# Optimization experiments

Measured on AMD Instinct MI355X. Metric: run time of the kernel, lower is better.

## Reference

```python
import jax, jax.numpy as jnp
import numpy as np

N, LT, LV, D, H = 4, 1024, 1024, 1024, 16
HD = D // H
EPS = 1e-12


def layernorm(x, w, b):
    u = x.mean(-1, keepdims=True)
    s = ((x - u) ** 2).mean(-1, keepdims=True)
    return w * (x - u) / jnp.sqrt(s + EPS) + b


def attention(q_in, k_in, v_in, mask, qw, qb, kw, kb, vw, vb):
    # mask: (N, Lq_or_1, Lk) float in {0,1}; torch Linear is x @ W.T + b
    def heads(x, w, b):
        y = x @ w.T + b
        return y.reshape(y.shape[0], y.shape[1], H, HD).transpose(0, 2, 1, 3)  # (N,H,L,hd)
    q, k, v = heads(q_in, qw, qb), heads(k_in, kw, kb), heads(v_in, vw, vb)
    scores = jnp.einsum('bhqd,bhkd->bhqk', q, k) / np.sqrt(HD).astype(np.float32)
    scores = scores + (1.0 - mask[:, None]) * (-10000.0)
    probs = jax.nn.softmax(scores, axis=-1)  # dropout is identity in eval
    ctx = jnp.einsum('bhqk,bhkd->bhqd', probs, v)
    return ctx.transpose(0, 2, 1, 3).reshape(q_in.shape[0], q_in.shape[1], D)


def setup_inputs() -> dict:
    key = jax.random.key(0)
    ks = jax.random.split(key, 16)
    inp = {
        'dec_hidden_states': jax.random.normal(ks[0], (N, LT, D), jnp.float32),
        'enc_outputs': jax.random.normal(ks[1], (N, LV, D), jnp.float32),
        'dec_mask': jnp.ones((N, LT), jnp.float32),
        'enc_mask': jnp.ones((N, LV), jnp.float32),
    }
    wnames = ['sa_qw', 'sa_kw', 'sa_vw', 'ca_qw', 'ca_kw', 'ca_vw', 'out_w']
    for i, n in enumerate(wnames):
        inp[n] = jax.random.normal(ks[2 + i], (D, D), jnp.float32) * 0.02
    for n in ['sa_qb', 'sa_kb', 'sa_vb', 'ca_qb', 'ca_kb', 'ca_vb', 'out_b', 'n1_b', 'n2_b', 'out_ln_b']:
        inp[n] = jnp.zeros((D,), jnp.float32)
    for n in ['n1_w', 'n2_w', 'out_ln_w']:
        inp[n] = jnp.ones((D,), jnp.float32)
    return inp


def reference(dec_hidden_states, enc_outputs, dec_mask, enc_mask,
              sa_qw, sa_qb, sa_kw, sa_kb, sa_vw, sa_vb, n1_w, n1_b,
              ca_qw, ca_qb, ca_kw, ca_kb, ca_vw, ca_vb, n2_w, n2_b,
              out_w, out_b, out_ln_w, out_ln_b):
    Lt = dec_mask.shape[1]
    # diagonal_mask=True: causal tril combined with padding mask
    self_mask = dec_mask[:, None, :] * jnp.tril(jnp.ones((Lt, Lt), dec_mask.dtype))  # (N,Lt,Lt)
    a = attention(dec_hidden_states, dec_hidden_states, dec_hidden_states, self_mask,
                  sa_qw, sa_qb, sa_kw, sa_kb, sa_vw, sa_vb)
    a = layernorm(a + dec_hidden_states, n1_w, n1_b)
    c = attention(a, enc_outputs, enc_outputs, enc_mask[:, None, :],
                  ca_qw, ca_qb, ca_kw, ca_kb, ca_vw, ca_vb)
    c = layernorm(a + c, n2_w, n2_b)
    # BertOutput called as output(x, x): dense, residual, LN (dropout = identity)
    h = c @ out_w.T + out_b
    return layernorm(h + c, out_ln_w, out_ln_b)
```

## Files before the change

kernel.cpp:

```cpp
#include <hip/hip_runtime.h>
#include <cstdint>
#include <cstddef>

typedef __bf16 bf16x8 __attribute__((ext_vector_type(8)));
typedef float  floatx4 __attribute__((ext_vector_type(4)));
typedef unsigned short ushortx8 __attribute__((ext_vector_type(8)));
typedef unsigned short ushortx4 __attribute__((ext_vector_type(4)));

#define MFMA16(a, b, c) __builtin_amdgcn_mfma_f32_16x16x32_bf16((a), (b), (c), 0, 0, 0)

__device__ inline unsigned short f2bf(float f) {
    unsigned int u = __float_as_uint(f);
    unsigned int r = (u + 0x7fffu + ((u >> 16) & 1u)) >> 16;
    return (unsigned short)r;
}

struct Src2 { const float* p[2]; };
__global__ __launch_bounds__(256) void k_x2_to_bf16(Src2 s2, unsigned short* __restrict__ dst) {
    int i = blockIdx.x * 256 + threadIdx.x;
    const float* src = s2.p[i >> 19];
    int off = i & 524287;
    const float4* s = (const float4*)src + (size_t)off * 2;
    float4 x0 = s[0], x1 = s[1];
    ushortx8 o;
    o[0] = f2bf(x0.x); o[1] = f2bf(x0.y); o[2] = f2bf(x0.z); o[3] = f2bf(x0.w);
    o[4] = f2bf(x1.x); o[5] = f2bf(x1.y); o[6] = f2bf(x1.z); o[7] = f2bf(x1.w);
    *((ushortx8*)dst + i) = o;
}
struct Src7 { const float* p[7]; };
__global__ __launch_bounds__(256) void k_w7_to_bf16(Src7 s7, unsigned short* __restrict__ dst) {
    int i = blockIdx.x * 256 + threadIdx.x;
    const float* src = s7.p[i >> 17];
    int off = i & 131071;
    const float4* s = (const float4*)src + (size_t)off * 2;
    float4 x0 = s[0], x1 = s[1];
    ushortx8 o;
    o[0] = f2bf(x0.x); o[1] = f2bf(x0.y); o[2] = f2bf(x0.z); o[3] = f2bf(x0.w);
    o[4] = f2bf(x1.x); o[5] = f2bf(x1.y); o[6] = f2bf(x1.z); o[7] = f2bf(x1.w);
    *((ushortx8*)dst + i) = o;
}

template <int MODE>
__global__ __launch_bounds__(256) void k_gemm_bias(const unsigned short* __restrict__ A,
                                                   const unsigned short* __restrict__ A2,
                                                   const unsigned short* __restrict__ W,
                                                   const float* __restrict__ bias0,
                                                   const float* __restrict__ bias1,
                                                   const float* __restrict__ bias2,
                                                   void* __restrict__ d0,
                                                   void* __restrict__ d1,
                                                   void* __restrict__ d2,
                                                   int K) {
    __shared__ __align__(16) unsigned short As[128 * 64];
    __shared__ __align__(16) unsigned short Bs[128 * 64];
    const int tid = threadIdx.x;
    const int wave = tid >> 6, lane = tid & 63;
    const int quad = lane >> 4, l15 = lane & 15;
    const int wm = wave >> 1, wn = wave & 1;

    constexpr int NT = (MODE == 3) ? 8 : 24;
    int fid = blockIdx.y * 32 + blockIdx.x;
    int xcd = fid & 7, idx = fid >> 3;
    const int m0 = (xcd * 4 + idx / NT) * 128;
    const int n0 = (idx % NT) * 128;
    const int sect_blk = n0 >> 10;

    const unsigned short* Ause = (MODE == 4 && sect_blk != 0) ? A2 : A;

    const size_t rowbytes = (size_t)K * 2;
    const int idx0 = tid, idx1 = 256 + tid;
    const char* pA0 = (const char*)Ause + (size_t)(m0 + (idx0 >> 2)) * rowbytes + ((idx0 & 3) << 4);
    const char* pA1 = (const char*)Ause + (size_t)(m0 + (idx1 >> 2)) * rowbytes + ((idx1 & 3) << 4);
    const char* pB0 = (const char*)W + (size_t)(n0 + (idx0 >> 2)) * rowbytes + ((idx0 & 3) << 4);
    const char* pB1 = (const char*)W + (size_t)(n0 + (idx1 >> 2)) * rowbytes + ((idx1 & 3) << 4);

    int4 a0a = *(const int4*)pA0, a0b = *(const int4*)(pA0 + 64);
    int4 a1a = *(const int4*)pA1, a1b = *(const int4*)(pA1 + 64);
    int4 b0a = *(const int4*)pB0, b0b = *(const int4*)(pB0 + 64);
    int4 b1a = *(const int4*)pB1, b1b = *(const int4*)(pB1 + 64);

    floatx4 acc[4][4] = {};

    const int KT = K >> 6;
    for (int kt = 0; kt < KT; ++kt) {
        __syncthreads();
        ((int4*)As)[idx0] = a0a; ((int4*)As)[idx1] = a1a;
        ((int4*)As)[512 + idx0] = a0b; ((int4*)As)[512 + idx1] = a1b;
        ((int4*)Bs)[idx0] = b0a; ((int4*)Bs)[idx1] = b1a;
        ((int4*)Bs)[512 + idx0] = b0b; ((int4*)Bs)[512 + idx1] = b1b;
        __syncthreads();
        if (kt + 1 < KT) {
            pA0 += 128; pA1 += 128; pB0 += 128; pB1 += 128;
            a0a = *(const int4*)pA0; a0b = *(const int4*)(pA0 + 64);
            a1a = *(const int4*)pA1; a1b = *(const int4*)(pA1 + 64);
            b0a = *(const int4*)pB0; b0b = *(const int4*)(pB0 + 64);
            b1a = *(const int4*)pB1; b1b = *(const int4*)(pB1 + 64);
        }
        const char* Asb = (const char*)As;
        const char* Bsb = (const char*)Bs;
#pragma unroll
        for (int half = 0; half < 2; ++half) {
            const int hb = half * 8192;
            bf16x8 af[4], bfr[4];
#pragma unroll
            for (int r = 0; r < 4; ++r)
                af[r] = *(const bf16x8*)(Asb + hb + ((wm * 64 + r * 16 + l15) * 64 + quad * 16));
#pragma unroll
            for (int c = 0; c < 4; ++c)
                bfr[c] = *(const bf16x8*)(Bsb + hb + ((wn * 64 + c * 16 + l15) * 64 + quad * 16));
#pragma unroll
            for (int r = 0; r < 4; ++r)
#pragma unroll
                for (int c = 0; c < 4; ++c)
                    acc[r][c] = MFMA16(af[r], bfr[c], acc[r][c]);
        }
    }

#pragma unroll
    for (int c = 0; c < 4; ++c) {
        int col = n0 + wn * 64 + c * 16 + l15;
        int sect = col >> 10, cc = col & 1023;
        float bv;
        if (MODE == 3) bv = bias0[col];
        else bv = (sect == 0 ? bias0 : (sect == 1 ? bias1 : bias2))[cc];
        int h = cc >> 6, d = cc & 63;
#pragma unroll
        for (int r = 0; r < 4; ++r) {
            int mrow = m0 + wm * 64 + r * 16 + quad * 4;
#pragma unroll
            for (int i = 0; i < 4; ++i) {
                float v = acc[r][c][i] + bv;
                int row = mrow + i;
                if (MODE == 3) {
                    ((float*)d0)[(size_t)row * 1024 + col] = v;
                } else {
                    int b = row >> 10, l = row & 1023;
                    unsigned short* base = (unsigned short*)(sect == 0 ? d0 : (sect == 1 ? d1 : d2));
                    bool isV = (sect == 2);
                    size_t off;
                    if (isV) {
                        int kk = l & 31;
                        off = (size_t)(b * 16 + h) * 65536 + (size_t)(l >> 5) * 2048 + d * 32 + kk;
                    } else {
                        off = ((size_t)(b * 16 + h) * 1024 + l) * 64 + d;
                    }
                    base[off] = f2bf(v);
                }
            }
        }
    }
}

__global__ __launch_bounds__(256, 4) void k_flash_attn(const unsigned short* __restrict__ Qp,
                                                       const unsigned short* __restrict__ Kp,
                                                       const unsigned short* __restrict__ Vp,
                                                       const float* __restrict__ mask,
                                                       float* __restrict__ ctx,
                                                       int causal) {
    const int L = 1024, D = 1024;
    const float SC = 0.18033688011112042f;
    int f = blockIdx.x;
    int g = f >> 7;
    int qsel = (f >> 3) & 15;
    int bh = (f & 7) + (g << 3);
    int qt = (qsel + 2 * g) & 15;
    int h = bh & 15, b = bh >> 4;
    int tid = threadIdx.x;
    int wave = tid >> 6, lane = tid & 63, quad = lane >> 4, l15 = lane & 15;
    int qbase = qt * 64 + wave * 16;

    __shared__ __align__(16) unsigned short Ks[2 * 4096];
    __shared__ __align__(16) unsigned short Vs[2 * 5120];
    __shared__ float penf[1024];

    {
        float4 mv = ((const float4*)(mask + b * L))[tid];
        float4 pv;
        pv.x = (1.0f - mv.x) * -14426.950408889634f;
        pv.y = (1.0f - mv.y) * -14426.950408889634f;
        pv.z = (1.0f - mv.z) * -14426.950408889634f;
        pv.w = (1.0f - mv.w) * -14426.950408889634f;
        ((float4*)penf)[tid] = pv;
    }

    const unsigned short* Qh = Qp + ((size_t)(b * 16 + h) * 1024 + qbase) * 64;
    bf16x8 qf0 = *(const bf16x8*)(Qh + l15 * 64 + quad * 8);
    bf16x8 qf1 = *(const bf16x8*)(Qh + l15 * 64 + 32 + quad * 8);

    const char* Kh = (const char*)(Kp + (size_t)(b * 16 + h) * 65536);
    const char* Vh = (const char*)(Vp + (size_t)(b * 16 + h) * 65536);

    int ktiles = causal ? (qt + 1) : 16;

    int krow = tid >> 3, kblk = tid & 7;
    int kd0 = krow * 128 + ((kblk ^ (krow & 7)) << 4);
    int kd1 = kd0 + 4096;
    int vd0 = (tid >> 2) * 80 + ((tid & 3) << 4);
    int vd1 = vd0 + 5120;

    int karA[4], karB[4];
#pragma unroll
    for (int r = 0; r < 4; ++r) {
        int row = r * 16 + l15;
        karA[r] = row * 128 + ((quad ^ (l15 & 7)) << 4);
        karB[r] = row * 128 + (((quad | 4) ^ (l15 & 7)) << 4);
    }
    int var_[8];
#pragma unroll
    for (int s = 0; s < 2; ++s)
#pragma unroll
        for (int fi = 0; fi < 4; ++fi)
            var_[s * 4 + fi] = s * 5120 + (fi * 16 + l15) * 80 + (quad << 4);

    floatx4 O[4] = {};
    float lsum = 0.0f;

    int4 ka0 = *(const int4*)(Kh + tid * 16);
    int4 ka1 = *(const int4*)(Kh + 4096 + tid * 16);
    int4 va0 = *(const int4*)(Vh + tid * 16);
    int4 va1 = *(const int4*)(Vh + 4096 + tid * 16);
    {
        char* Kw = (char*)Ks;
        char* Vw = (char*)Vs;
        *(int4*)(Kw + kd0) = ka0;
        *(int4*)(Kw + kd1) = ka1;
        *(int4*)(Vw + vd0) = va0;
        *(int4*)(Vw + vd1) = va1;
    }
    __syncthreads();

    for (int kt = 0; kt < ktiles; ++kt) {
        const char* Ksb = (const char*)Ks + (size_t)(kt & 1) * 8192;
        const char* Vsb = (const char*)Vs + (size_t)(kt & 1) * 10240;
        int k0 = kt * 64;
        bool last = (kt + 1 >= ktiles);

        bf16x8 kA[4], kB[4];
#pragma unroll
        for (int r = 0; r < 4; ++r) {
            kA[r] = *(const bf16x8*)(Ksb + karA[r]);
            kB[r] = *(const bf16x8*)(Ksb + karB[r]);
        }
        bf16x8 vv[8];
#pragma unroll
        for (int s = 0; s < 8; ++s) vv[s] = *(const bf16x8*)(Vsb + var_[s]);

        if (!last) {
            const char* Kg = Kh + (size_t)(kt + 1) * 8192;
            const char* Vg = Vh + (size_t)(kt + 1) * 8192;
            ka0 = *(const int4*)(Kg + tid * 16);
            ka1 = *(const int4*)(Kg + 4096 + tid * 16);
            va0 = *(const int4*)(Vg + tid * 16);
            va1 = *(const int4*)(Vg + 4096 + tid * 16);
        }

        floatx4 T[4] = {};
        T[0] = MFMA16(kA[0], qf0, T[0]); T[0] = MFMA16(kB[0], qf1, T[0]);
        T[1] = MFMA16(kA[1], qf0, T[1]); T[1] = MFMA16(kB[1], qf1, T[1]);
        T[2] = MFMA16(kA[2], qf0, T[2]); T[2] = MFMA16(kB[2], qf1, T[2]);
        T[3] = MFMA16(kA[3], qf0, T[3]); T[3] = MFMA16(kB[3], qf1, T[3]);

        bool boundary = causal && (kt == ktiles - 1);
        int qv = qbase + l15;

        unsigned w_[4][2];
#pragma unroll
        for (int s = 0; s < 4; ++s) {
            floatx4 pr = *(const floatx4*)(penf + k0 + 16 * s + quad * 4);
            unsigned rr[4];
#pragma unroll
            for (int i = 0; i < 4; ++i) {
                float x = fmaf(T[s][i], SC, pr[i]);
                if (boundary) {
                    int key = k0 + 16 * s + quad * 4 + i;
                    x = (key <= qv) ? x : -50000.0f;
                }
                float p = __builtin_amdgcn_exp2f(x);
                lsum += p;
                rr[i] = __float_as_uint(p) + 0x8000u;
            }
            w_[s][0] = __builtin_amdgcn_perm(rr[1], rr[0], 0x07060302u);
            w_[s][1] = __builtin_amdgcn_perm(rr[3], rr[2], 0x07060302u);
        }

        unsigned a00 = w_[0][0], a10 = w_[1][0];
        unsigned a01 = w_[0][1], a11 = w_[1][1];
        unsigned a20 = w_[2][0], a30 = w_[3][0];
        unsigned a21 = w_[2][1], a31 = w_[3][1];
        asm("v_permlane32_swap_b32 %0, %1" : "+v"(a00), "+v"(a10));
        asm("v_permlane32_swap_b32 %0, %1" : "+v"(a01), "+v"(a11));
        asm("v_permlane32_swap_b32 %0, %1" : "+v"(a20), "+v"(a30));
        asm("v_permlane32_swap_b32 %0, %1" : "+v"(a21), "+v"(a31));
        asm("v_permlane16_swap_b32 %0, %1" : "+v"(a00), "+v"(a10));
        asm("v_permlane16_swap_b32 %0, %1" : "+v"(a01), "+v"(a11));
        asm("v_permlane16_swap_b32 %0, %1" : "+v"(a20), "+v"(a30));
        asm("v_permlane16_swap_b32 %0, %1" : "+v"(a21), "+v"(a31));
        union PU { unsigned u[4]; bf16x8 v; };
        PU pl, ph;
        pl.u[0] = a00; pl.u[1] = a01; pl.u[2] = a10; pl.u[3] = a11;
        ph.u[0] = a20; ph.u[1] = a21; ph.u[2] = a30; ph.u[3] = a31;

        O[0] = MFMA16(pl.v, vv[0], O[0]);
        O[1] = MFMA16(pl.v, vv[1], O[1]);
        O[2] = MFMA16(pl.v, vv[2], O[2]);
        O[3] = MFMA16(pl.v, vv[3], O[3]);
        O[0] = MFMA16(ph.v, vv[4], O[0]);
        O[1] = MFMA16(ph.v, vv[5], O[1]);
        O[2] = MFMA16(ph.v, vv[6], O[2]);
        O[3] = MFMA16(ph.v, vv[7], O[3]);

        if (!last) {
            char* Kw = (char*)Ks + (size_t)((kt + 1) & 1) * 8192;
            char* Vw = (char*)Vs + (size_t)((kt + 1) & 1) * 10240;
            *(int4*)(Kw + kd0) = ka0;
            *(int4*)(Kw + kd1) = ka1;
            *(int4*)(Vw + vd0) = va0;
            *(int4*)(Vw + vd1) = va1;
        }
        __syncthreads();
    }

    lsum += __shfl_xor(lsum, 16);
    lsum += __shfl_xor(lsum, 32);
#pragma unroll
    for (int i = 0; i < 4; ++i) {
        float lt = __shfl(lsum, quad * 4 + i);
        float inv = 1.0f / lt;
        int qi = qbase + quad * 4 + i;
        float* op = ctx + ((size_t)(b * L + qi)) * D + h * 64;
#pragma unroll
        for (int fi = 0; fi < 4; ++fi) op[fi * 16 + l15] = O[fi][i] * inv;
    }
}

__global__ __launch_bounds__(256) void k_add_ln(const float* __restrict__ X,
                                                const float* __restrict__ Y,
                                                const float* __restrict__ w,
                                                const float* __restrict__ bvec,
                                                float* __restrict__ outf,
                                                unsigned short* __restrict__ outbf) {
    int row = blockIdx.x;
    int tid = threadIdx.x;
    float4 x = *((const float4*)(X + (size_t)row * 1024) + tid);
    float4 y = *((const float4*)(Y + (size_t)row * 1024) + tid);
    float v0 = x.x + y.x, v1 = x.y + y.y, v2 = x.z + y.z, v3 = x.w + y.w;
    float s = v0 + v1 + v2 + v3;
    float s2 = v0 * v0 + v1 * v1 + v2 * v2 + v3 * v3;
#pragma unroll
    for (int off = 32; off > 0; off >>= 1) {
        s += __shfl_xor(s, off);
        s2 += __shfl_xor(s2, off);
    }
    __shared__ float red[8];
    int wave = tid >> 6, lane = tid & 63;
    if (lane == 0) { red[wave] = s; red[4 + wave] = s2; }
    __syncthreads();
    s = red[0] + red[1] + red[2] + red[3];
    s2 = red[4] + red[5] + red[6] + red[7];
    float u = s * (1.0f / 1024.0f);
    float var = s2 * (1.0f / 1024.0f) - u * u;
    float r = 1.0f / sqrtf(fmaxf(var, 0.0f) + 1e-12f);
    float4 wv = *((const float4*)w + tid);
    float4 bv = *((const float4*)bvec + tid);
    float o0 = wv.x * (v0 - u) * r + bv.x;
    float o1 = wv.y * (v1 - u) * r + bv.y;
    float o2 = wv.z * (v2 - u) * r + bv.z;
    float o3 = wv.w * (v3 - u) * r + bv.w;
    float4 o = {o0, o1, o2, o3};
    *((float4*)(outf + (size_t)row * 1024) + tid) = o;
    if (outbf) {
        ushortx4 ob;
        ob[0] = f2bf(o0); ob[1] = f2bf(o1); ob[2] = f2bf(o2); ob[3] = f2bf(o3);
        *((ushortx4*)outbf + (size_t)row * 256 + tid) = ob;
    }
}

extern "C" void kernel_launch(void* const* d_in, const int* in_sizes, int n_in,
                              void* d_out, int out_size, void* d_ws, size_t ws_size,
                              hipStream_t stream) {
    (void)in_sizes; (void)n_in; (void)out_size; (void)ws_size;
    const float* dec = (const float*)d_in[0];
    const float* enc = (const float*)d_in[1];
    const float* dec_mask = (const float*)d_in[2];
    const float* enc_mask = (const float*)d_in[3];
    const float* b_saq = (const float*)d_in[11];
    const float* b_sak = (const float*)d_in[12];
    const float* b_sav = (const float*)d_in[13];
    const float* b_caq = (const float*)d_in[14];
    const float* b_cak = (const float*)d_in[15];
    const float* b_cav = (const float*)d_in[16];
    const float* b_out = (const float*)d_in[17];
    const float* n1_b = (const float*)d_in[18];
    const float* n2_b = (const float*)d_in[19];
    const float* oln_b = (const float*)d_in[20];
    const float* n1_w = (const float*)d_in[21];
    const float* n2_w = (const float*)d_in[22];
    const float* oln_w = (const float*)d_in[23];

    char* ws = (char*)d_ws;
    const size_t MB2 = 2097152;
    const size_t ACT_BF = 8388608;
    const size_t ACT_F32 = 16777216;
    unsigned short* Wbf[7];
    for (int i = 0; i < 7; ++i) Wbf[i] = (unsigned short*)(ws + i * MB2);
    size_t off = 7 * MB2;
    unsigned short* Xbf = (unsigned short*)(ws + off); off += ACT_BF;
    unsigned short* Ebf = (unsigned short*)(ws + off); off += ACT_BF;
    unsigned short* Abf = (unsigned short*)(ws + off); off += ACT_BF;
    unsigned short* Cbf = (unsigned short*)(ws + off); off += ACT_BF;
    unsigned short* Qp = (unsigned short*)(ws + off); off += ACT_BF;
    unsigned short* Kp = (unsigned short*)(ws + off); off += ACT_BF;
    unsigned short* Vp = (unsigned short*)(ws + off); off += ACT_BF;
    float* ctx = (float*)(ws + off); off += ACT_F32;
    float* a_f32 = (float*)(ws + off); off += ACT_F32;
    float* c_f32 = (float*)(ws + off); off += ACT_F32;
    float* h_f32 = ctx;
    float* outp = (float*)d_out;

    dim3 blk(256);
    dim3 attn_grid(1024);

    Src2 s2; s2.p[0] = dec; s2.p[1] = enc;
    k_x2_to_bf16<<<dim3(4096), blk, 0, stream>>>(s2, Xbf);
    Src7 s7;
    for (int i = 0; i < 7; ++i) s7.p[i] = (const float*)d_in[4 + i];
    k_w7_to_bf16<<<dim3(3584), blk, 0, stream>>>(s7, Wbf[0]);

    k_gemm_bias<0><<<dim3(32, 24), blk, 0, stream>>>(Xbf, Xbf, Wbf[0], b_saq, b_sak, b_sav,
                                                     Qp, Kp, Vp, 1024);
    k_flash_attn<<<attn_grid, blk, 0, stream>>>(Qp, Kp, Vp, dec_mask, ctx, 1);
    k_add_ln<<<dim3(4096), blk, 0, stream>>>(ctx, dec, n1_w, n1_b, a_f32, Abf);

    k_gemm_bias<4><<<dim3(32, 24), blk, 0, stream>>>(Abf, Ebf, Wbf[3], b_caq, b_cak, b_cav,
                                                     Qp, Kp, Vp, 1024);
    k_flash_attn<<<attn_grid, blk, 0, stream>>>(Qp, Kp, Vp, enc_mask, ctx, 0);
    k_add_ln<<<dim3(4096), blk, 0, stream>>>(a_f32, ctx, n2_w, n2_b, c_f32, Cbf);

    k_gemm_bias<3><<<dim3(32, 8), blk, 0, stream>>>(Cbf, Cbf, Wbf[6], b_out, b_out, b_out,
                                                    h_f32, nullptr, nullptr, 1024);
    k_add_ln<<<dim3(4096), blk, 0, stream>>>(h_f32, c_f32, oln_w, oln_b, outp, (unsigned short*)nullptr);
}
```

Baseline: 329.4 us.

## Load K/V fragments directly from global memory in flash attention, dropping LDS staging

The attention kernel no longer stages K and V tiles through double-buffered shared memory. Each wave now reads its MFMA fragments straight from global memory (through L1/L2), which removes the per-tile __syncthreads and the LDS write/read traffic. MFMA blocks are also wrapped in s_setprio to favour matrix issue. The risk is that four waves now load the same K/V data redundantly and there is no explicit prefetch, so global-load latency is exposed inside the loop.

Measured after the change: 410.8 us. +24.7%, slower.

```diff
diff --git a/kernel.cpp b/kernel.cpp
--- a/kernel.cpp
+++ b/kernel.cpp
@@ -169,8 +169,6 @@
     int wave = tid >> 6, lane = tid & 63, quad = lane >> 4, l15 = lane & 15;
     int qbase = qt * 64 + wave * 16;
 
-    __shared__ __align__(16) unsigned short Ks[2 * 4096];
-    __shared__ __align__(16) unsigned short Vs[2 * 5120];
     __shared__ float penf[1024];
 
     {
@@ -182,6 +180,7 @@
         pv.w = (1.0f - mv.w) * -14426.950408889634f;
         ((float4*)penf)[tid] = pv;
     }
+    __syncthreads();
 
     const unsigned short* Qh = Qp + ((size_t)(b * 16 + h) * 1024 + qbase) * 64;
     bf16x8 qf0 = *(const bf16x8*)(Qh + l15 * 64 + quad * 8);
@@ -192,76 +191,39 @@
 
     int ktiles = causal ? (qt + 1) : 16;
 
-    int krow = tid >> 3, kblk = tid & 7;
-    int kd0 = krow * 128 + ((kblk ^ (krow & 7)) << 4);
-    int kd1 = kd0 + 4096;
-    int vd0 = (tid >> 2) * 80 + ((tid & 3) << 4);
-    int vd1 = vd0 + 5120;
-
-    int karA[4], karB[4];
-#pragma unroll
-    for (int r = 0; r < 4; ++r) {
-        int row = r * 16 + l15;
-        karA[r] = row * 128 + ((quad ^ (l15 & 7)) << 4);
-        karB[r] = row * 128 + (((quad | 4) ^ (l15 & 7)) << 4);
-    }
-    int var_[8];
-#pragma unroll
-    for (int s = 0; s < 2; ++s)
-#pragma unroll
-        for (int fi = 0; fi < 4; ++fi)
-            var_[s * 4 + fi] = s * 5120 + (fi * 16 + l15) * 80 + (quad << 4);
-
     floatx4 O[4] = {};
     float lsum = 0.0f;
-
-    int4 ka0 = *(const int4*)(Kh + tid * 16);
-    int4 ka1 = *(const int4*)(Kh + 4096 + tid * 16);
-    int4 va0 = *(const int4*)(Vh + tid * 16);
-    int4 va1 = *(const int4*)(Vh + 4096 + tid * 16);
-    {
-        char* Kw = (char*)Ks;
-        char* Vw = (char*)Vs;
-        *(int4*)(Kw + kd0) = ka0;
-        *(int4*)(Kw + kd1) = ka1;
-        *(int4*)(Vw + vd0) = va0;
-        *(int4*)(Vw + vd1) = va1;
-    }
-    __syncthreads();
+    int qv = qbase + l15;
 
     for (int kt = 0; kt < ktiles; ++kt) {
-        const char* Ksb = (const char*)Ks + (size_t)(kt & 1) * 8192;
-        const char* Vsb = (const char*)Vs + (size_t)(kt & 1) * 10240;
+        const char* Kt = Kh + (size_t)kt * 8192;
+        const char* Vt = Vh + (size_t)kt * 8192;
         int k0 = kt * 64;
-        bool last = (kt + 1 >= ktiles);
 
         bf16x8 kA[4], kB[4];
 #pragma unroll
         for (int r = 0; r < 4; ++r) {
-            kA[r] = *(const bf16x8*)(Ksb + karA[r]);
-            kB[r] = *(const bf16x8*)(Ksb + karB[r]);
-        }
-        bf16x8 vv[8];
-#pragma unroll
-        for (int s = 0; s < 8; ++s) vv[s] = *(const bf16x8*)(Vsb + var_[s]);
-
-        if (!last) {
-            const char* Kg = Kh + (size_t)(kt + 1) * 8192;
-            const char* Vg = Vh + (size_t)(kt + 1) * 8192;
-            ka0 = *(const int4*)(Kg + tid * 16);
-            ka1 = *(const int4*)(Kg + 4096 + tid * 16);
-            va0 = *(const int4*)(Vg + tid * 16);
-            va1 = *(const int4*)(Vg + 4096 + tid * 16);
+            const char* rowp = Kt + (r * 16 + l15) * 128;
+            kA[r] = *(const bf16x8*)(rowp + quad * 16);
+            kB[r] = *(const bf16x8*)(rowp + 64 + quad * 16);
         }
 
         floatx4 T[4] = {};
+        __builtin_amdgcn_s_setprio(1);
         T[0] = MFMA16(kA[0], qf0, T[0]); T[0] = MFMA16(kB[0], qf1, T[0]);
         T[1] = MFMA16(kA[1], qf0, T[1]); T[1] = MFMA16(kB[1], qf1, T[1]);
         T[2] = MFMA16(kA[2], qf0, T[2]); T[2] = MFMA16(kB[2], qf1, T[2]);
         T[3] = MFMA16(kA[3], qf0, T[3]); T[3] = MFMA16(kB[3], qf1, T[3]);
+        __builtin_amdgcn_s_setprio(0);
+
+        bf16x8 vv[8];
+#pragma unroll
+        for (int s = 0; s < 2; ++s)
+#pragma unroll
+            for (int fi = 0; fi < 4; ++fi)
+                vv[s * 4 + fi] = *(const bf16x8*)(Vt + s * 4096 + (fi * 16 + l15) * 64 + quad * 16);
 
         bool boundary = causal && (kt == ktiles - 1);
-        int qv = qbase + l15;
 
         unsigned w_[4][2];
 #pragma unroll
@@ -300,6 +262,7 @@
         pl.u[0] = a00; pl.u[1] = a01; pl.u[2] = a10; pl.u[3] = a11;
         ph.u[0] = a20; ph.u[1] = a21; ph.u[2] = a30; ph.u[3] = a31;
 
+        __builtin_amdgcn_s_setprio(1);
         O[0] = MFMA16(pl.v, vv[0], O[0]);
         O[1] = MFMA16(pl.v, vv[1], O[1]);
         O[2] = MFMA16(pl.v, vv[2], O[2]);
@@ -308,16 +271,7 @@
         O[1] = MFMA16(ph.v, vv[5], O[1]);
         O[2] = MFMA16(ph.v, vv[6], O[2]);
         O[3] = MFMA16(ph.v, vv[7], O[3]);
-
-        if (!last) {
-            char* Kw = (char*)Ks + (size_t)((kt + 1) & 1) * 8192;
-            char* Vw = (char*)Vs + (size_t)((kt + 1) & 1) * 10240;
-            *(int4*)(Kw + kd0) = ka0;
-            *(int4*)(Kw + kd1) = ka1;
-            *(int4*)(Vw + vd0) = va0;
-            *(int4*)(Vw + vd1) = va1;
-        }
-        __syncthreads();
+        __builtin_amdgcn_s_setprio(0);
     }
 
     lsum += __shfl_xor(lsum, 16);
```

## Double query tile per attention block and merge conversion kernels

Applied to the files above, without the earlier changes.

The flash attention kernel now processes 128 query rows per block, 32 per wave as two 16-row halves. Each staged K/V tile is therefore reused across twice as many queries, and the grid shrinks to 512 blocks. Causal masking skips fully masked halves and tiles per wave, and the occupancy hint is lowered from 4 to 2 blocks per CU to allow more registers. The activation and weight fp32-to-bf16 conversion kernels are fused into one launch. The risks are fewer blocks to balance the causal workload and higher register pressure.

Measured after the change: 330.3 us. About the same (+0.3%).

```diff
diff --git a/kernel.cpp b/kernel.cpp
--- a/kernel.cpp
+++ b/kernel.cpp
@@ -15,29 +15,31 @@
     return (unsigned short)r;
 }
 
-struct Src2 { const float* p[2]; };
-__global__ __launch_bounds__(256) void k_x2_to_bf16(Src2 s2, unsigned short* __restrict__ dst) {
-    int i = blockIdx.x * 256 + threadIdx.x;
-    const float* src = s2.p[i >> 19];
-    int off = i & 524287;
-    const float4* s = (const float4*)src + (size_t)off * 2;
-    float4 x0 = s[0], x1 = s[1];
-    ushortx8 o;
-    o[0] = f2bf(x0.x); o[1] = f2bf(x0.y); o[2] = f2bf(x0.z); o[3] = f2bf(x0.w);
-    o[4] = f2bf(x1.x); o[5] = f2bf(x1.y); o[6] = f2bf(x1.z); o[7] = f2bf(x1.w);
-    *((ushortx8*)dst + i) = o;
-}
-struct Src7 { const float* p[7]; };
-__global__ __launch_bounds__(256) void k_w7_to_bf16(Src7 s7, unsigned short* __restrict__ dst) {
-    int i = blockIdx.x * 256 + threadIdx.x;
-    const float* src = s7.p[i >> 17];
-    int off = i & 131071;
-    const float4* s = (const float4*)src + (size_t)off * 2;
-    float4 x0 = s[0], x1 = s[1];
-    ushortx8 o;
-    o[0] = f2bf(x0.x); o[1] = f2bf(x0.y); o[2] = f2bf(x0.z); o[3] = f2bf(x0.w);
-    o[4] = f2bf(x1.x); o[5] = f2bf(x1.y); o[6] = f2bf(x1.z); o[7] = f2bf(x1.w);
-    *((ushortx8*)dst + i) = o;
+struct SrcAll { const float* a[2]; const float* w[7]; };
+__global__ __launch_bounds__(256) void k_conv(SrcAll s, unsigned short* __restrict__ adst,
+                                              unsigned short* __restrict__ wdst) {
+    int bid = blockIdx.x;
+    if (bid < 4096) {
+        int i = bid * 256 + threadIdx.x;
+        const float* src = s.a[i >> 19];
+        int off = i & 524287;
+        const float4* p = (const float4*)src + (size_t)off * 2;
+        float4 x0 = p[0], x1 = p[1];
+        ushortx8 o;
+        o[0] = f2bf(x0.x); o[1] = f2bf(x0.y); o[2] = f2bf(x0.z); o[3] = f2bf(x0.w);
+        o[4] = f2bf(x1.x); o[5] = f2bf(x1.y); o[6] = f2bf(x1.z); o[7] = f2bf(x1.w);
+        *((ushortx8*)adst + i) = o;
+    } else {
+        int i = (bid - 4096) * 256 + threadIdx.x;
+        const float* src = s.w[i >> 17];
+        int off = i & 131071;
+        const float4* p = (const float4*)src + (size_t)off * 2;
+        float4 x0 = p[0], x1 = p[1];
+        ushortx8 o;
+        o[0] = f2bf(x0.x); o[1] = f2bf(x0.y); o[2] = f2bf(x0.z); o[3] = f2bf(x0.w);
+        o[4] = f2bf(x1.x); o[5] = f2bf(x1.y); o[6] = f2bf(x1.z); o[7] = f2bf(x1.w);
+        *((ushortx8*)wdst + i) = o;
+    }
 }
 
 template <int MODE>
@@ -151,7 +153,7 @@
     }
 }
 
-__global__ __launch_bounds__(256, 4) void k_flash_attn(const unsigned short* __restrict__ Qp,
+__global__ __launch_bounds__(256, 2) void k_flash_attn(const unsigned short* __restrict__ Qp,
                                                        const unsigned short* __restrict__ Kp,
                                                        const unsigned short* __restrict__ Vp,
                                                        const float* __restrict__ mask,
@@ -160,14 +162,13 @@
     const int L = 1024, D = 1024;
     const float SC = 0.18033688011112042f;
     int f = blockIdx.x;
-    int g = f >> 7;
-    int qsel = (f >> 3) & 15;
+    int g = f >> 6;
     int bh = (f & 7) + (g << 3);
-    int qt = (qsel + 2 * g) & 15;
+    int qt = ((f >> 3) + g) & 7;
     int h = bh & 15, b = bh >> 4;
     int tid = threadIdx.x;
     int wave = tid >> 6, lane = tid & 63, quad = lane >> 4, l15 = lane & 15;
-    int qbase = qt * 64 + wave * 16;
+    int qbase = qt * 128 + wave * 32;
 
     __shared__ __align__(16) unsigned short Ks[2 * 4096];
     __shared__ __align__(16) unsigned short Vs[2 * 5120];
@@ -184,13 +185,17 @@
     }
 
     const unsigned short* Qh = Qp + ((size_t)(b * 16 + h) * 1024 + qbase) * 64;
-    bf16x8 qf0 = *(const bf16x8*)(Qh + l15 * 64 + quad * 8);
-    bf16x8 qf1 = *(const bf16x8*)(Qh + l15 * 64 + 32 + quad * 8);
+    bf16x8 qf[2][2];
+#pragma unroll
+    for (int qh = 0; qh < 2; ++qh) {
+        qf[qh][0] = *(const bf16x8*)(Qh + (qh * 16 + l15) * 64 + quad * 8);
+        qf[qh][1] = *(const bf16x8*)(Qh + (qh * 16 + l15) * 64 + 32 + quad * 8);
+    }
 
     const char* Kh = (const char*)(Kp + (size_t)(b * 16 + h) * 65536);
     const char* Vh = (const char*)(Vp + (size_t)(b * 16 + h) * 65536);
 
-    int ktiles = causal ? (qt + 1) : 16;
+    int ktiles = causal ? (2 * qt + 2) : 16;
 
     int krow = tid >> 3, kblk = tid & 7;
     int kd0 = krow * 128 + ((kblk ^ (krow & 7)) << 4);
@@ -212,8 +217,8 @@
         for (int fi = 0; fi < 4; ++fi)
             var_[s * 4 + fi] = s * 5120 + (fi * 16 + l15) * 80 + (quad << 4);
 
-    floatx4 O[4] = {};
-    float lsum = 0.0f;
+    floatx4 O[2][4] = {};
+    float lsum[2] = {0.0f, 0.0f};
 
     int4 ka0 = *(const int4*)(Kh + tid * 16);
     int4 ka1 = *(const int4*)(Kh + 4096 + tid * 16);
@@ -234,16 +239,18 @@
         const char* Vsb = (const char*)Vs + (size_t)(kt & 1) * 10240;
         int k0 = kt * 64;
         bool last = (kt + 1 >= ktiles);
-
-        bf16x8 kA[4], kB[4];
-#pragma unroll
-        for (int r = 0; r < 4; ++r) {
-            kA[r] = *(const bf16x8*)(Ksb + karA[r]);
-            kB[r] = *(const bf16x8*)(Ksb + karB[r]);
-        }
-        bf16x8 vv[8];
-#pragma unroll
-        for (int s = 0; s < 8; ++s) vv[s] = *(const bf16x8*)(Vsb + var_[s]);
+        bool vis = !(causal && k0 > qbase + 31);
+
+        bf16x8 kA[4], kB[4], vv[8];
+        if (vis) {
+#pragma unroll
+            for (int r = 0; r < 4; ++r) {
+                kA[r] = *(const bf16x8*)(Ksb + karA[r]);
+                kB[r] = *(const bf16x8*)(Ksb + karB[r]);
+            }
+#pragma unroll
+            for (int s = 0; s < 8; ++s) vv[s] = *(const bf16x8*)(Vsb + var_[s]);
+        }
 
         if (!last) {
             const char* Kg = Kh + (size_t)(kt + 1) * 8192;
@@ -254,60 +261,67 @@
             va1 = *(const int4*)(Vg + 4096 + tid * 16);
         }
 
-        floatx4 T[4] = {};
-        T[0] = MFMA16(kA[0], qf0, T[0]); T[0] = MFMA16(kB[0], qf1, T[0]);
-        T[1] = MFMA16(kA[1], qf0, T[1]); T[1] = MFMA16(kB[1], qf1, T[1]);
-        T[2] = MFMA16(kA[2], qf0, T[2]); T[2] = MFMA16(kB[2], qf1, T[2]);
-        T[3] = MFMA16(kA[3], qf0, T[3]); T[3] = MFMA16(kB[3], qf1, T[3]);
-
-        bool boundary = causal && (kt == ktiles - 1);
-        int qv = qbase + l15;
-
-        unsigned w_[4][2];
-#pragma unroll
-        for (int s = 0; s < 4; ++s) {
-            floatx4 pr = *(const floatx4*)(penf + k0 + 16 * s + quad * 4);
-            unsigned rr[4];
-#pragma unroll
-            for (int i = 0; i < 4; ++i) {
-                float x = fmaf(T[s][i], SC, pr[i]);
-                if (boundary) {
-                    int key = k0 + 16 * s + quad * 4 + i;
-                    x = (key <= qv) ? x : -50000.0f;
+        if (vis) {
+#pragma unroll
+            for (int qh = 0; qh < 2; ++qh) {
+                int qlo = qbase + qh * 16;
+                if (causal && k0 > qlo + 15) continue;
+                bool boundary = causal && (k0 + 63 > qlo);
+                int qv = qlo + l15;
+
+                floatx4 T[4] = {};
+                T[0] = MFMA16(kA[0], qf[qh][0], T[0]); T[0] = MFMA16(kB[0], qf[qh][1], T[0]);
+                T[1] = MFMA16(kA[1], qf[qh][0], T[1]); T[1] = MFMA16(kB[1], qf[qh][1], T[1]);
+                T[2] = MFMA16(kA[2], qf[qh][0], T[2]); T[2] = MFMA16(kB[2], qf[qh][1], T[2]);
+                T[3] = MFMA16(kA[3], qf[qh][0], T[3]); T[3] = MFMA16(kB[3], qf[qh][1], T[3]);
+
+                unsigned w_[4][2];
+#pragma unroll
+                for (int s = 0; s < 4; ++s) {
+                    floatx4 pr = *(const floatx4*)(penf + k0 + 16 * s + quad * 4);
+                    unsigned rr[4];
+#pragma unroll
+                    for (int i = 0; i < 4; ++i) {
+                        float x = fmaf(T[s][i], SC, pr[i]);
+                        if (boundary) {
+                            int key = k0 + 16 * s + quad * 4 + i;
+                            x = (key <= qv) ? x : -50000.0f;
+                        }
+                        float p = __builtin_amdgcn_exp2f(x);
+                        lsum[qh] += p;
+                        rr[i] = __float_as_uint(p) + 0x8000u;
+                    }
+                    w_[s][0] = __builtin_amdgcn_perm(rr[1], rr[0], 0x07060302u);
+                    w_[s][1] = __builtin_amdgcn_perm(rr[3], rr[2], 0x07060302u);
                 }
-                float p = __builtin_amdgcn_exp2f(x);
-                lsum += p;
-                rr[i] = __float_as_uint(p) + 0x8000u;
+
+                unsigned a00 = w_[0][0], a10 = w_[1][0];
+                unsigned a01 = w_[0][1], a11 = w_[1][1];
+                unsigned a20 = w_[2][0], a30 = w_[3][0];
+                unsigned a21 = w_[2][1], a31 = w_[3][1];
+                asm("v_permlane32_swap_b32 %0, %1" : "+v"(a00), "+v"(a10));
+                asm("v_permlane32_swap_b32 %0, %1" : "+v"(a01), "+v"(a11));
+                asm("v_permlane32_swap_b32 %0, %1" : "+v"(a20), "+v"(a30));
+                asm("v_permlane32_swap_b32 %0, %1" : "+v"(a21), "+v"(a31));
+                asm("v_permlane16_swap_b32 %0, %1" : "+v"(a00), "+v"(a10));
+                asm("v_permlane16_swap_b32 %0, %1" : "+v"(a01), "+v"(a11));
+                asm("v_permlane16_swap_b32 %0, %1" : "+v"(a20), "+v"(a30));
+                asm("v_permlane16_swap_b32 %0, %1" : "+v"(a21), "+v"(a31));
+                union PU { unsigned u[4]; bf16x8 v; };
+                PU pl, ph;
+                pl.u[0] = a00; pl.u[1] = a01; pl.u[2] = a10; pl.u[3] = a11;
+                ph.u[0] = a20; ph.u[1] = a21; ph.u[2] = a30; ph.u[3] = a31;
+
+                O[qh][0] = MFMA16(pl.v, vv[0], O[qh][0]);
+                O[qh][1] = MFMA16(pl.v, vv[1], O[qh][1]);
+                O[qh][2] = MFMA16(pl.v, vv[2], O[qh][2]);
+                O[qh][3] = MFMA16(pl.v, vv[3], O[qh][3]);
+                O[qh][0] = MFMA16(ph.v, vv[4], O[qh][0]);
+                O[qh][1] = MFMA16(ph.v, vv[5], O[qh][1]);
+                O[qh][2] = MFMA16(ph.v, vv[6], O[qh][2]);
+                O[qh][3] = MFMA16(ph.v, vv[7], O[qh][3]);
             }
-            w_[s][0] = __builtin_amdgcn_perm(rr[1], rr[0], 0x07060302u);
-            w_[s][1] = __builtin_amdgcn_perm(rr[3], rr[2], 0x07060302u);
-        }
-
-        unsigned a00 = w_[0][0], a10 = w_[1][0];
-        unsigned a01 = w_[0][1], a11 = w_[1][1];
-        unsigned a20 = w_[2][0], a30 = w_[3][0];
-        unsigned a21 = w_[2][1], a31 = w_[3][1];
-        asm("v_permlane32_swap_b32 %0, %1" : "+v"(a00), "+v"(a10));
-        asm("v_permlane32_swap_b32 %0, %1" : "+v"(a01), "+v"(a11));
-        asm("v_permlane32_swap_b32 %0, %1" : "+v"(a20), "+v"(a30));
-        asm("v_permlane32_swap_b32 %0, %1" : "+v"(a21), "+v"(a31));
-        asm("v_permlane16_swap_b32 %0, %1" : "+v"(a00), "+v"(a10));
-        asm("v_permlane16_swap_b32 %0, %1" : "+v"(a01), "+v"(a11));
-        asm("v_permlane16_swap_b32 %0, %1" : "+v"(a20), "+v"(a30));
-        asm("v_permlane16_swap_b32 %0, %1" : "+v"(a21), "+v"(a31));
-        union PU { unsigned u[4]; bf16x8 v; };
-        PU pl, ph;
-        pl.u[0] = a00; pl.u[1] = a01; pl.u[2] = a10; pl.u[3] = a11;
-        ph.u[0] = a20; ph.u[1] = a21; ph.u[2] = a30; ph.u[3] = a31;
-
-        O[0] = MFMA16(pl.v, vv[0], O[0]);
-        O[1] = MFMA16(pl.v, vv[1], O[1]);
-        O[2] = MFMA16(pl.v, vv[2], O[2]);
-        O[3] = MFMA16(pl.v, vv[3], O[3]);
-        O[0] = MFMA16(ph.v, vv[4], O[0]);
-        O[1] = MFMA16(ph.v, vv[5], O[1]);
-        O[2] = MFMA16(ph.v, vv[6], O[2]);
-        O[3] = MFMA16(ph.v, vv[7], O[3]);
+        }
 
         if (!last) {
             char* Kw = (char*)Ks + (size_t)((kt + 1) & 1) * 8192;
@@ -320,16 +334,20 @@
         __syncthreads();
     }
 
-    lsum += __shfl_xor(lsum, 16);
-    lsum += __shfl_xor(lsum, 32);
-#pragma unroll
-    for (int i = 0; i < 4; ++i) {
-        float lt = __shfl(lsum, quad * 4 + i);
-        float inv = 1.0f / lt;
-        int qi = qbase + quad * 4 + i;
-        float* op = ctx + ((size_t)(b * L + qi)) * D + h * 64;
-#pragma unroll
-        for (int fi = 0; fi < 4; ++fi) op[fi * 16 + l15] = O[fi][i] * inv;
+#pragma unroll
+    for (int qh = 0; qh < 2; ++qh) {
+        float ls = lsum[qh];
+        ls += __shfl_xor(ls, 16);
+        ls += __shfl_xor(ls, 32);
+#pragma unroll
+        for (int i = 0; i < 4; ++i) {
+            float lt = __shfl(ls, quad * 4 + i);
+            float inv = 1.0f / lt;
+            int qi = qbase + qh * 16 + quad * 4 + i;
+            float* op = ctx + ((size_t)(b * L + qi)) * D + h * 64;
+#pragma unroll
+            for (int fi = 0; fi < 4; ++fi) op[fi * 16 + l15] = O[qh][fi][i] * inv;
+        }
     }
 }
 
@@ -418,13 +436,12 @@
     float* outp = (float*)d_out;
 
     dim3 blk(256);
-    dim3 attn_grid(1024);
-
-    Src2 s2; s2.p[0] = dec; s2.p[1] = enc;
-    k_x2_to_bf16<<<dim3(4096), blk, 0, stream>>>(s2, Xbf);
-    Src7 s7;
-    for (int i = 0; i < 7; ++i) s7.p[i] = (const float*)d_in[4 + i];
-    k_w7_to_bf16<<<dim3(3584), blk, 0, stream>>>(s7, Wbf[0]);
+    dim3 attn_grid(512);
+
+    SrcAll sa;
+    sa.a[0] = dec; sa.a[1] = enc;
+    for (int i = 0; i < 7; ++i) sa.w[i] = (const float*)d_in[4 + i];
+    k_conv<<<dim3(7680), blk, 0, stream>>>(sa, Xbf, Wbf[0]);
 
     k_gemm_bias<0><<<dim3(32, 24), blk, 0, stream>>>(Xbf, Xbf, Wbf[0], b_saq, b_sak, b_sav,
                                                      Qp, Kp, Vp, 1024);
```
